# Optimization experiments

Measured on AMD Instinct MI355X. Metric: run time of the kernel, lower is better.

## Reference

```python
import jax, jax.numpy as jnp
import numpy as np

IN_SIZE = 1024
HIDDEN = 1024
BATCH = 4096


def _linear_params(key, out_dim, in_dim):
    # torch nn.Linear init: U(-1/sqrt(in_dim), 1/sqrt(in_dim)) for W and b
    k1, k2 = jax.random.split(key)
    bound = 1.0 / np.sqrt(in_dim)
    W = jax.random.uniform(k1, (out_dim, in_dim), jnp.float32, -bound, bound)
    b = jax.random.uniform(k2, (out_dim,), jnp.float32, -bound, bound)
    return W, b


def setup_inputs() -> dict:
    key = jax.random.key(0)
    keys = jax.random.split(key, 11)
    x = jax.random.normal(keys[0], (BATCH, IN_SIZE), jnp.float32)
    hidden = jax.random.normal(keys[1], (BATCH, HIDDEN), jnp.float32)
    cell = jax.random.normal(keys[2], (BATCH, HIDDEN), jnp.float32)
    names = ['xf', 'xi', 'xo', 'xc', 'hf', 'hi', 'ho', 'hc']
    inp = {'x': x, 'hidden': hidden, 'cell': cell}
    for n, k in zip(names, keys[3:]):
        in_dim = IN_SIZE if n[0] == 'x' else HIDDEN
        W, b = _linear_params(k, HIDDEN, in_dim)
        inp['W_' + n] = W
        inp['b_' + n] = b
    return inp


def reference(x, hidden, cell,
              W_xf, b_xf, W_xi, b_xi, W_xo, b_xo, W_xc, b_xc,
              W_hf, b_hf, W_hi, b_hi, W_ho, b_ho, W_hc, b_hc):
    # gates: sigmoid/tanh over (x-linear + h-linear) pairs
    f = jax.nn.sigmoid(x @ W_xf.T + b_xf + hidden @ W_hf.T + b_hf)
    i = jax.nn.sigmoid(x @ W_xi.T + b_xi + hidden @ W_hi.T + b_hi)
    o = jax.nn.sigmoid(x @ W_xo.T + b_xo + hidden @ W_ho.T + b_ho)
    c = jnp.tanh(x @ W_xc.T + b_xc + hidden @ W_hc.T + b_hc)
    updated_cell = f * cell + i * c
    updated_hidden = o * jnp.tanh(updated_cell)
    return updated_hidden, updated_cell
```

## Files before the change

### kernel.cpp

```cpp
#include <hip/hip_runtime.h>
#include <hip/hip_bf16.h>

#define BATCH 4096
#define NH    1024
#define KCAT  2048
#define NJ    4096
#define NT    (KCAT / 64)

typedef __bf16 bf16x8 __attribute__((ext_vector_type(8)));
typedef float  f32x4  __attribute__((ext_vector_type(4)));
typedef unsigned short u16x8 __attribute__((ext_vector_type(8)));

struct WPtrs { const float* wx[4]; const float* wh[4]; };
struct BPtrs { const float* bx[4]; const float* bh[4]; };

__device__ __forceinline__ unsigned short f2b(float f) {
  union { float f; unsigned u; } v; v.f = f;
  return (unsigned short)((v.u + 0x7fffu + ((v.u >> 16) & 1u)) >> 16);
}

__device__ __forceinline__ void gload_lds16(const void* g, void* l) {
  __builtin_amdgcn_global_load_lds(
      (const __attribute__((address_space(1))) unsigned int*)g,
      (__attribute__((address_space(3))) unsigned int*)l, 16, 0, 0);
}

__device__ __forceinline__ float sigmoid_f(float x) {
  x = fminf(fmaxf(x, -30.f), 30.f);
  return 1.f / (1.f + __expf(-x));
}
__device__ __forceinline__ float tanh_f(float x) {
  x = fminf(fmaxf(x, -15.f), 15.f);
  float e = __expf(2.f * x);
  return (e - 1.f) / (e + 1.f);
}

__global__ __launch_bounds__(256) void pack_all(
    const float* __restrict__ x, const float* __restrict__ h,
    WPtrs W, BPtrs B,
    __hip_bfloat16* __restrict__ Acat, __hip_bfloat16* __restrict__ Bcat,
    float* __restrict__ biasc) {
  int bid = blockIdx.x;
  if (bid < 4096) {
    int t = bid * 256 + threadIdx.x;
    int base = t * 8;
    int row = base >> 11;
    int k   = base & 2047;
    const float* src = (k < 1024) ? (x + (size_t)row * 1024 + k)
                                  : (h + (size_t)row * 1024 + (k - 1024));
    float4 v0 = ((const float4*)src)[0];
    float4 v1 = ((const float4*)src)[1];
    u16x8 o;
    o[0]=f2b(v0.x); o[1]=f2b(v0.y); o[2]=f2b(v0.z); o[3]=f2b(v0.w);
    o[4]=f2b(v1.x); o[5]=f2b(v1.y); o[6]=f2b(v1.z); o[7]=f2b(v1.w);
    *(u16x8*)((unsigned short*)Acat + base) = o;
  } else if (bid < 8192) {
    int t = (bid - 4096) * 256 + threadIdx.x;
    int base = t * 8;
    int j = base >> 11;
    int k = base & 2047;
    int n = ((j >> 6) << 4) + (j & 15);
    int g = (j >> 4) & 3;
    const float* src = (k < 1024) ? (W.wx[g] + (size_t)n * 1024 + k)
                                  : (W.wh[g] + (size_t)n * 1024 + (k - 1024));
    float4 v0 = ((const float4*)src)[0];
    float4 v1 = ((const float4*)src)[1];
    u16x8 o;
    o[0]=f2b(v0.x); o[1]=f2b(v0.y); o[2]=f2b(v0.z); o[3]=f2b(v0.w);
    o[4]=f2b(v1.x); o[5]=f2b(v1.y); o[6]=f2b(v1.z); o[7]=f2b(v1.w);
    *(u16x8*)((unsigned short*)Bcat + base) = o;
  } else {
    int i = (bid - 8192) * 256 + threadIdx.x;
    int g = i >> 10, n = i & 1023;
    biasc[i] = B.bx[g][n] + B.bh[g][n];
  }
}


#define STAGE_A_HALF(T, H)                                                      \
  {                                                                             \
    _Pragma("unroll")                                                           \
    for (int i_ = 0; i_ < 2; ++i_) {                                            \
      gload_lds16(Ag + (size_t)((H)*128 + i_*64 + strow) * KCAT + (T)*64 +      \
                      stchnk * 8,                                               \
                  &smem[((T)&1)*32768 + (H)*8192 + i_*4096 + w*512]);           \
    }                                                                           \
  }
#define STAGE_B_HALF(T, H)                                                      \
  {                                                                             \
    _Pragma("unroll")                                                           \
    for (int i_ = 0; i_ < 2; ++i_) {                                            \
      gload_lds16(Bg + (size_t)((H)*128 + i_*64 + strow) * KCAT + (T)*64 +      \
                      stchnk * 8,                                               \
                  &smem[((T)&1)*32768 + 16384 + (H)*8192 + i_*4096 + w*512]);   \
    }                                                                           \
  }
#define STAGE_A_SLICE(T, S)                                                     \
  {                                                                             \
    gload_lds16(Ag + (size_t)(arbw + (S)*32 + (lane >> 3)) * KCAT + (T)*64 +    \
                    stchnk * 8,                                                 \
                &smem[((T)&1)*32768 + (arbw + (S)*32) * 64]);                   \
  }

__global__ __launch_bounds__(512, 2) void lstm_gemm8(
    const unsigned short* __restrict__ Acat,
    const unsigned short* __restrict__ Bcat,
    const float* __restrict__ biasc,
    const float* __restrict__ cell,
    float* __restrict__ outH, float* __restrict__ outC) {
  __shared__ unsigned short smem[65536];

  const int tid  = threadIdx.x;
  const int w    = tid >> 6;
  const int lane = tid & 63;
  const int wr   = w >> 2;
  const int wc   = w & 3;
  const int lr   = lane & 15;
  const int cb0  = ((lane >> 4) & 3) * 16;
  const int sx   = (lr & 7) << 4;

  const int bid = blockIdx.x;
  const int s   = (bid & 7) * 32 + (bid >> 3);
  const int bx  = s & 15;
  const int by  = s >> 4;

  const unsigned short* Ag = Acat + (size_t)(by * 256) * KCAT;
  const unsigned short* Bg = Bcat + (size_t)(bx * 256) * KCAT;

  const int strow  = w * 8 + (lane >> 3);
  const int stchnk = (lane & 7) ^ ((lane >> 3) & 7);
  const int arbw   = (w >> 2) * 128 + (w & 3) * 8;

  const int arow0 = (wr * 128 + lr) * 128;
  const int brow0 = 32768 + (wc * 64 + lr) * 128;
  const int colb0 = cb0 ^ sx;
  const int colb1 = (64 + cb0) ^ sx;
  const char* smc = (const char*)smem;

  const int n_out = (bx * 4 + wc) * 16 + lr;
  const float bfv = biasc[n_out];
  const float biv = biasc[1024 + n_out];
  const float bov = biasc[2048 + n_out];
  const float bcv = biasc[3072 + n_out];

  f32x4 acc[8][4] = {};

  STAGE_A_HALF(0, 0);
  STAGE_A_HALF(0, 1);
  STAGE_B_HALF(0, 0);
  STAGE_B_HALF(0, 1);
  STAGE_A_SLICE(1, 0);
  STAGE_A_SLICE(1, 1);
  STAGE_A_SLICE(1, 2);
  STAGE_B_HALF(1, 0);
  STAGE_B_HALF(1, 1);
  asm volatile("s_waitcnt vmcnt(7)" ::: "memory");
  __builtin_amdgcn_sched_barrier(0);
  __builtin_amdgcn_s_barrier();

  for (int t = 0; t < NT; ++t) {
    const int cur  = t & 1;
    const int curo = cur * 65536;
    bf16x8 bfr[4][2];
#pragma unroll
    for (int p = 0; p < 4; ++p) {
      bf16x8 af[2][2];
#pragma unroll
      for (int mi = 0; mi < 2; ++mi) {
        af[mi][0] = *(const bf16x8*)(smc + curo + arow0 + (2*p+mi)*2048 + colb0);
        af[mi][1] = *(const bf16x8*)(smc + curo + arow0 + (2*p+mi)*2048 + colb1);
      }
      if (p == 0) {
#pragma unroll
        for (int n = 0; n < 4; ++n) {
          bfr[n][0] = *(const bf16x8*)(smc + curo + brow0 + n*2048 + colb0);
          bfr[n][1] = *(const bf16x8*)(smc + curo + brow0 + n*2048 + colb1);
        }
      }
      if (p == 0 && t + 1 < NT) STAGE_A_SLICE(t + 1, 3);
      if (p == 1 && t + 2 < NT) { STAGE_A_SLICE(t + 2, 0); STAGE_B_HALF(t + 2, 0); }
      if (p == 2 && t + 2 < NT) { STAGE_A_SLICE(t + 2, 1); STAGE_B_HALF(t + 2, 1); }
      if (p == 3 && t + 2 < NT) STAGE_A_SLICE(t + 2, 2);
      if (p == 0) asm volatile("s_waitcnt lgkmcnt(8)" ::: "memory");
      __builtin_amdgcn_sched_barrier(0);
      __builtin_amdgcn_s_barrier();
      asm volatile("s_waitcnt lgkmcnt(0)" ::: "memory");
      __builtin_amdgcn_sched_barrier(0);
      __builtin_amdgcn_s_setprio(1);
#pragma unroll
      for (int mi = 0; mi < 2; ++mi)
#pragma unroll
        for (int n = 0; n < 4; ++n) {
          acc[2*p+mi][n] = __builtin_amdgcn_mfma_f32_16x16x32_bf16(
              af[mi][0], bfr[n][0], acc[2*p+mi][n], 0, 0, 0);
          acc[2*p+mi][n] = __builtin_amdgcn_mfma_f32_16x16x32_bf16(
              af[mi][1], bfr[n][1], acc[2*p+mi][n], 0, 0, 0);
        }
      __builtin_amdgcn_s_setprio(0);
      if (p == 3) {
        if (t < NT - 2) {
          asm volatile("s_waitcnt vmcnt(7)" ::: "memory");
        } else if (t == NT - 2) {
          asm volatile("s_waitcnt vmcnt(0)" ::: "memory");
        }
        __builtin_amdgcn_sched_barrier(0);
      }
      __builtin_amdgcn_s_barrier();
    }
  }

  const int q0 = (lane >> 4) * 4;
#pragma unroll
  for (int m = 0; m < 8; ++m) {
    int row0 = by * 256 + wr * 128 + m * 16 + q0;
#pragma unroll
    for (int q = 0; q < 4; ++q) {
      int row = row0 + q;
      float pf = acc[m][0][q] + bfv;
      float pi = acc[m][1][q] + biv;
      float po = acc[m][2][q] + bov;
      float pc = acc[m][3][q] + bcv;
      float fg = sigmoid_f(pf);
      float ig = sigmoid_f(pi);
      float og = sigmoid_f(po);
      float cg = tanh_f(pc);
      float cold = cell[(size_t)row * NH + n_out];
      float cn = fg * cold + ig * cg;
      float hn = og * tanh_f(cn);
      outH[(size_t)row * NH + n_out] = hn;
      outC[(size_t)row * NH + n_out] = cn;
    }
  }
}

extern "C" void kernel_launch(void* const* d_in, const int* in_sizes, int n_in,
                              void* d_out, int out_size, void* d_ws, size_t ws_size,
                              hipStream_t stream) {
  const float* x    = (const float*)d_in[0];
  const float* h    = (const float*)d_in[1];
  const float* cell = (const float*)d_in[2];
  WPtrs wp; BPtrs bp;
  for (int g = 0; g < 4; ++g) {
    wp.wx[g] = (const float*)d_in[3 + 2 * g];
    bp.bx[g] = (const float*)d_in[4 + 2 * g];
    wp.wh[g] = (const float*)d_in[11 + 2 * g];
    bp.bh[g] = (const float*)d_in[12 + 2 * g];
  }

  char* ws = (char*)d_ws;
  __hip_bfloat16* Acat = (__hip_bfloat16*)ws;
  __hip_bfloat16* Bcat = (__hip_bfloat16*)(ws + (size_t)BATCH * KCAT * 2);
  float* biasc = (float*)(ws + (size_t)BATCH * KCAT * 2 + (size_t)NJ * KCAT * 2);

  float* outH = (float*)d_out;
  float* outC = outH + (size_t)BATCH * NH;

  pack_all<<<8208, 256, 0, stream>>>(x, h, wp, bp, Acat, Bcat, biasc);

  lstm_gemm8<<<256, 512, 0, stream>>>((const unsigned short*)Acat,
                                      (const unsigned short*)Bcat,
                                      biasc, cell, outH, outC);
}
```

Measured before the change: 88.01 us.

## Double-buffer A fragments in registers to overlap LDS reads with MFMA

Adds a two-slot register buffer for A fragments so the next phase's LDS reads are issued before the current phase's MFMAs, including a cross-tile prefetch from the next shared-memory buffer after the barrier. The waitcnt schedule is reworked: the vmcnt wait moves before the last A-slice stage, and lgkmcnt waits now let the prefetch stay in flight. Bias loads move after the main loop to shorten register live ranges. This raises VGPR pressure under 512-thread, 2-block launch bounds, which could cause spills or reduced occupancy.

```diff
diff --git a/kernel.cpp b/kernel.cpp
--- a/kernel.cpp
+++ b/kernel.cpp
@@ -102,6 +102,11 @@
                 &smem[((T)&1)*32768 + (arbw + (S)*32) * 64]);                   \
   }
 
+#define LDA_(BUFO, MP, KH)                                                      \
+  (*(const bf16x8*)(smc + (BUFO) + arow0 + (MP)*2048 + ((KH) ? colb1 : colb0)))
+#define LDB_(BUFO, N, KH)                                                       \
+  (*(const bf16x8*)(smc + (BUFO) + brow0 + (N)*2048 + ((KH) ? colb1 : colb0)))
+
 __global__ __launch_bounds__(512, 2) void lstm_gemm8(
     const unsigned short* __restrict__ Acat,
     const unsigned short* __restrict__ Bcat,
@@ -137,13 +142,9 @@
   const int colb1 = (64 + cb0) ^ sx;
   const char* smc = (const char*)smem;
 
-  const int n_out = (bx * 4 + wc) * 16 + lr;
-  const float bfv = biasc[n_out];
-  const float biv = biasc[1024 + n_out];
-  const float bov = biasc[2048 + n_out];
-  const float bcv = biasc[3072 + n_out];
-
   f32x4 acc[8][4] = {};
+  bf16x8 af[2][2][2];
+  bf16x8 bfr[4][2];
 
   STAGE_A_HALF(0, 0);
   STAGE_A_HALF(0, 1);
@@ -157,34 +158,61 @@
   asm volatile("s_waitcnt vmcnt(7)" ::: "memory");
   __builtin_amdgcn_sched_barrier(0);
   __builtin_amdgcn_s_barrier();
+#pragma unroll
+  for (int mi = 0; mi < 2; ++mi) {
+    af[0][mi][0] = LDA_(0, mi, 0);
+    af[0][mi][1] = LDA_(0, mi, 1);
+  }
 
   for (int t = 0; t < NT; ++t) {
-    const int cur  = t & 1;
-    const int curo = cur * 65536;
-    bf16x8 bfr[4][2];
+    const int curo = (t & 1) * 65536;
+    const int nxto = curo ^ 65536;
 #pragma unroll
     for (int p = 0; p < 4; ++p) {
-      bf16x8 af[2][2];
-#pragma unroll
-      for (int mi = 0; mi < 2; ++mi) {
-        af[mi][0] = *(const bf16x8*)(smc + curo + arow0 + (2*p+mi)*2048 + colb0);
-        af[mi][1] = *(const bf16x8*)(smc + curo + arow0 + (2*p+mi)*2048 + colb1);
-      }
+      const int cs = p & 1;
+      const int ns = cs ^ 1;
       if (p == 0) {
 #pragma unroll
         for (int n = 0; n < 4; ++n) {
-          bfr[n][0] = *(const bf16x8*)(smc + curo + brow0 + n*2048 + colb0);
-          bfr[n][1] = *(const bf16x8*)(smc + curo + brow0 + n*2048 + colb1);
+          bfr[n][0] = LDB_(curo, n, 0);
+          bfr[n][1] = LDB_(curo, n, 1);
+        }
+      }
+      if (p < 3) {
+#pragma unroll
+        for (int mi = 0; mi < 2; ++mi) {
+          af[ns][mi][0] = LDA_(curo, 2*(p+1)+mi, 0);
+          af[ns][mi][1] = LDA_(curo, 2*(p+1)+mi, 1);
         }
       }
       if (p == 0 && t + 1 < NT) STAGE_A_SLICE(t + 1, 3);
       if (p == 1 && t + 2 < NT) { STAGE_A_SLICE(t + 2, 0); STAGE_B_HALF(t + 2, 0); }
       if (p == 2 && t + 2 < NT) { STAGE_A_SLICE(t + 2, 1); STAGE_B_HALF(t + 2, 1); }
-      if (p == 3 && t + 2 < NT) STAGE_A_SLICE(t + 2, 2);
-      if (p == 0) asm volatile("s_waitcnt lgkmcnt(8)" ::: "memory");
+      if (p == 3) {
+        if (t < NT - 2) {
+          asm volatile("s_waitcnt vmcnt(6)" ::: "memory");
+        } else if (t == NT - 2) {
+          asm volatile("s_waitcnt vmcnt(0)" ::: "memory");
+        }
+        __builtin_amdgcn_sched_barrier(0);
+        if (t + 2 < NT) STAGE_A_SLICE(t + 2, 2);
+      }
       __builtin_amdgcn_sched_barrier(0);
       __builtin_amdgcn_s_barrier();
-      asm volatile("s_waitcnt lgkmcnt(0)" ::: "memory");
+      if (p == 3) {
+        if (t + 1 < NT) {
+#pragma unroll
+          for (int mi = 0; mi < 2; ++mi) {
+            af[ns][mi][0] = LDA_(nxto, mi, 0);
+            af[ns][mi][1] = LDA_(nxto, mi, 1);
+          }
+          asm volatile("s_waitcnt lgkmcnt(4)" ::: "memory");
+        } else {
+          asm volatile("s_waitcnt lgkmcnt(0)" ::: "memory");
+        }
+      } else {
+        asm volatile("s_waitcnt lgkmcnt(4)" ::: "memory");
+      }
       __builtin_amdgcn_sched_barrier(0);
       __builtin_amdgcn_s_setprio(1);
 #pragma unroll
@@ -192,24 +220,22 @@
 #pragma unroll
         for (int n = 0; n < 4; ++n) {
           acc[2*p+mi][n] = __builtin_amdgcn_mfma_f32_16x16x32_bf16(
-              af[mi][0], bfr[n][0], acc[2*p+mi][n], 0, 0, 0);
+              af[cs][mi][0], bfr[n][0], acc[2*p+mi][n], 0, 0, 0);
           acc[2*p+mi][n] = __builtin_amdgcn_mfma_f32_16x16x32_bf16(
-              af[mi][1], bfr[n][1], acc[2*p+mi][n], 0, 0, 0);
+              af[cs][mi][1], bfr[n][1], acc[2*p+mi][n], 0, 0, 0);
         }
       __builtin_amdgcn_s_setprio(0);
-      if (p == 3) {
-        if (t < NT - 2) {
-          asm volatile("s_waitcnt vmcnt(7)" ::: "memory");
-        } else if (t == NT - 2) {
-          asm volatile("s_waitcnt vmcnt(0)" ::: "memory");
-        }
-        __builtin_amdgcn_sched_barrier(0);
-      }
       __builtin_amdgcn_s_barrier();
     }
   }
 
+  const int n_out = (bx * 4 + wc) * 16 + lr;
+  const float bfv = biasc[n_out];
+  const float biv = biasc[1024 + n_out];
+  const float bov = biasc[2048 + n_out];
+  const float bcv = biasc[3072 + n_out];
   const int q0 = (lane >> 4) * 4;
+
 #pragma unroll
   for (int m = 0; m < 8; ++m) {
     int row0 = by * 256 + wr * 128 + m * 16 + q0;
```

After: 87.56 us. Within noise of the previous version (-0.5%).

## Software-pipeline LDS fragment loads one phase ahead of MFMAs in GEMM loop

Applied to the files above, without the earlier changes.

Restructures the K-loop so that A fragments for the next quarter are read from LDS while the current quarter's MFMAs run, using a double-buffered af register set and finer lgkmcnt waits. The per-phase barriers and global prefetch issue points are reordered, and the vmcnt threshold moves to match. Bias loads are moved after the main loop to shorten register live ranges. This aims to hide LDS read latency behind matrix math, at the cost of more live VGPRs and a fragile hand-tuned wait schedule.

```diff
diff --git a/kernel.cpp b/kernel.cpp
--- a/kernel.cpp
+++ b/kernel.cpp
@@ -102,6 +102,21 @@
                 &smem[((T)&1)*32768 + (arbw + (S)*32) * 64]);                   \
   }
 
+#define LDA_(BUFO, MP, KH)                                                      \
+  (*(const bf16x8*)(smc + (BUFO) + arow0 + (MP)*2048 + ((KH) ? colb1 : colb0)))
+#define LDB_(BUFO, N, KH)                                                       \
+  (*(const bf16x8*)(smc + (BUFO) + brow0 + (N)*2048 + ((KH) ? colb1 : colb0)))
+
+#define MFMA_HALF(BASE, SET, KH)                                                \
+  {                                                                             \
+    _Pragma("unroll")                                                           \
+    for (int mi_ = 0; mi_ < 2; ++mi_)                                           \
+      _Pragma("unroll")                                                         \
+      for (int n_ = 0; n_ < 4; ++n_)                                            \
+        acc[(BASE)+mi_][n_] = __builtin_amdgcn_mfma_f32_16x16x32_bf16(          \
+            af[SET][mi_][KH], bfr[n_][KH], acc[(BASE)+mi_][n_], 0, 0, 0);       \
+  }
+
 __global__ __launch_bounds__(512, 2) void lstm_gemm8(
     const unsigned short* __restrict__ Acat,
     const unsigned short* __restrict__ Bcat,
@@ -137,13 +152,9 @@
   const int colb1 = (64 + cb0) ^ sx;
   const char* smc = (const char*)smem;
 
-  const int n_out = (bx * 4 + wc) * 16 + lr;
-  const float bfv = biasc[n_out];
-  const float biv = biasc[1024 + n_out];
-  const float bov = biasc[2048 + n_out];
-  const float bcv = biasc[3072 + n_out];
-
   f32x4 acc[8][4] = {};
+  bf16x8 af[2][2][2];
+  bf16x8 bfr[4][2];
 
   STAGE_A_HALF(0, 0);
   STAGE_A_HALF(0, 1);
@@ -159,57 +170,81 @@
   __builtin_amdgcn_s_barrier();
 
   for (int t = 0; t < NT; ++t) {
-    const int cur  = t & 1;
-    const int curo = cur * 65536;
-    bf16x8 bfr[4][2];
-#pragma unroll
-    for (int p = 0; p < 4; ++p) {
-      bf16x8 af[2][2];
-#pragma unroll
-      for (int mi = 0; mi < 2; ++mi) {
-        af[mi][0] = *(const bf16x8*)(smc + curo + arow0 + (2*p+mi)*2048 + colb0);
-        af[mi][1] = *(const bf16x8*)(smc + curo + arow0 + (2*p+mi)*2048 + colb1);
-      }
-      if (p == 0) {
-#pragma unroll
-        for (int n = 0; n < 4; ++n) {
-          bfr[n][0] = *(const bf16x8*)(smc + curo + brow0 + n*2048 + colb0);
-          bfr[n][1] = *(const bf16x8*)(smc + curo + brow0 + n*2048 + colb1);
-        }
-      }
-      if (p == 0 && t + 1 < NT) STAGE_A_SLICE(t + 1, 3);
-      if (p == 1 && t + 2 < NT) { STAGE_A_SLICE(t + 2, 0); STAGE_B_HALF(t + 2, 0); }
-      if (p == 2 && t + 2 < NT) { STAGE_A_SLICE(t + 2, 1); STAGE_B_HALF(t + 2, 1); }
-      if (p == 3 && t + 2 < NT) STAGE_A_SLICE(t + 2, 2);
-      if (p == 0) asm volatile("s_waitcnt lgkmcnt(8)" ::: "memory");
-      __builtin_amdgcn_sched_barrier(0);
-      __builtin_amdgcn_s_barrier();
-      asm volatile("s_waitcnt lgkmcnt(0)" ::: "memory");
-      __builtin_amdgcn_sched_barrier(0);
-      __builtin_amdgcn_s_setprio(1);
-#pragma unroll
-      for (int mi = 0; mi < 2; ++mi)
-#pragma unroll
-        for (int n = 0; n < 4; ++n) {
-          acc[2*p+mi][n] = __builtin_amdgcn_mfma_f32_16x16x32_bf16(
-              af[mi][0], bfr[n][0], acc[2*p+mi][n], 0, 0, 0);
-          acc[2*p+mi][n] = __builtin_amdgcn_mfma_f32_16x16x32_bf16(
-              af[mi][1], bfr[n][1], acc[2*p+mi][n], 0, 0, 0);
-        }
-      __builtin_amdgcn_s_setprio(0);
-      if (p == 3) {
-        if (t < NT - 2) {
-          asm volatile("s_waitcnt vmcnt(7)" ::: "memory");
-        } else if (t == NT - 2) {
-          asm volatile("s_waitcnt vmcnt(0)" ::: "memory");
-        }
-        __builtin_amdgcn_sched_barrier(0);
-      }
-      __builtin_amdgcn_s_barrier();
+    const int curo = (t & 1) * 65536;
+
+    af[0][0][0] = LDA_(curo, 0, 0); af[0][0][1] = LDA_(curo, 0, 1);
+    af[0][1][0] = LDA_(curo, 1, 0); af[0][1][1] = LDA_(curo, 1, 1);
+    __builtin_amdgcn_sched_barrier(0);
+    bfr[0][0] = LDB_(curo, 0, 0); bfr[1][0] = LDB_(curo, 1, 0);
+    bfr[2][0] = LDB_(curo, 2, 0); bfr[3][0] = LDB_(curo, 3, 0);
+    __builtin_amdgcn_sched_barrier(0);
+    bfr[0][1] = LDB_(curo, 0, 1); bfr[1][1] = LDB_(curo, 1, 1);
+    bfr[2][1] = LDB_(curo, 2, 1); bfr[3][1] = LDB_(curo, 3, 1);
+    __builtin_amdgcn_sched_barrier(0);
+    if (t + 1 < NT) STAGE_A_SLICE(t + 1, 3);
+    af[1][0][0] = LDA_(curo, 2, 0); af[1][0][1] = LDA_(curo, 2, 1);
+    af[1][1][0] = LDA_(curo, 3, 0); af[1][1][1] = LDA_(curo, 3, 1);
+    __builtin_amdgcn_sched_barrier(0);
+    __builtin_amdgcn_s_setprio(1);
+    asm volatile("s_waitcnt lgkmcnt(8)" ::: "memory");
+    __builtin_amdgcn_sched_barrier(0);
+    MFMA_HALF(0, 0, 0);
+    asm volatile("s_waitcnt lgkmcnt(4)" ::: "memory");
+    __builtin_amdgcn_sched_barrier(0);
+    MFMA_HALF(0, 0, 1);
+    __builtin_amdgcn_s_setprio(0);
+    __builtin_amdgcn_s_barrier();
+
+    af[0][0][0] = LDA_(curo, 4, 0); af[0][0][1] = LDA_(curo, 4, 1);
+    af[0][1][0] = LDA_(curo, 5, 0); af[0][1][1] = LDA_(curo, 5, 1);
+    __builtin_amdgcn_sched_barrier(0);
+    if (t + 2 < NT) { STAGE_A_SLICE(t + 2, 0); STAGE_B_HALF(t + 2, 0); }
+    __builtin_amdgcn_sched_barrier(0);
+    __builtin_amdgcn_s_setprio(1);
+    asm volatile("s_waitcnt lgkmcnt(4)" ::: "memory");
+    __builtin_amdgcn_sched_barrier(0);
+    MFMA_HALF(2, 1, 0);
+    MFMA_HALF(2, 1, 1);
+    __builtin_amdgcn_s_setprio(0);
+    __builtin_amdgcn_s_barrier();
+
+    af[1][0][0] = LDA_(curo, 6, 0); af[1][0][1] = LDA_(curo, 6, 1);
+    af[1][1][0] = LDA_(curo, 7, 0); af[1][1][1] = LDA_(curo, 7, 1);
+    __builtin_amdgcn_sched_barrier(0);
+    if (t + 2 < NT) { STAGE_A_SLICE(t + 2, 1); STAGE_B_HALF(t + 2, 1); }
+    __builtin_amdgcn_sched_barrier(0);
+    __builtin_amdgcn_s_setprio(1);
+    asm volatile("s_waitcnt lgkmcnt(4)" ::: "memory");
+    __builtin_amdgcn_sched_barrier(0);
+    MFMA_HALF(4, 0, 0);
+    MFMA_HALF(4, 0, 1);
+    __builtin_amdgcn_s_setprio(0);
+    __builtin_amdgcn_s_barrier();
+
+    if (t < NT - 2) {
+      asm volatile("s_waitcnt vmcnt(6)" ::: "memory");
+    } else if (t == NT - 2) {
+      asm volatile("s_waitcnt vmcnt(0)" ::: "memory");
     }
-  }
-
+    __builtin_amdgcn_sched_barrier(0);
+    if (t + 2 < NT) STAGE_A_SLICE(t + 2, 2);
+    __builtin_amdgcn_sched_barrier(0);
+    __builtin_amdgcn_s_setprio(1);
+    asm volatile("s_waitcnt lgkmcnt(0)" ::: "memory");
+    __builtin_amdgcn_sched_barrier(0);
+    MFMA_HALF(6, 1, 0);
+    MFMA_HALF(6, 1, 1);
+    __builtin_amdgcn_s_setprio(0);
+    __builtin_amdgcn_s_barrier();
+  }
+
+  const int n_out = (bx * 4 + wc) * 16 + lr;
+  const float bfv = biasc[n_out];
+  const float biv = biasc[1024 + n_out];
+  const float bov = biasc[2048 + n_out];
+  const float bcv = biasc[3072 + n_out];
   const int q0 = (lane >> 4) * 4;
+
 #pragma unroll
   for (int m = 0; m < 8; ++m) {
     int row0 = by * 256 + wr * 128 + m * 16 + q0;
```

Result: faster. 85.93 us (-2.4%).

## Restructure GEMM main loop into quadrant-based 8-phase ping-pong schedule

Applied to the files above, without the earlier changes.

Replaces the per-k-tile loop of four row-pair phases with a manually unrolled two-tile iteration. Each tile is split into four MFMA quadrants (4 M-fragments by 2 N-fragments), with LDS fragment reads and global-to-LDS staging of A and B halves interleaved between barriers. A is now staged in halves instead of 32-row slices, and the prologue no longer prefetches A for the next tile. The intent is better balance between LDS reads, global loads and MFMA work per barrier phase. In exchange it adds more barriers, a different vmcnt accounting that must be exactly right, and higher register use for the fragment arrays.

```diff
diff --git a/kernel.cpp b/kernel.cpp
--- a/kernel.cpp
+++ b/kernel.cpp
@@ -6,6 +6,7 @@
 #define KCAT  2048
 #define NJ    4096
 #define NT    (KCAT / 64)
+#define NIT   (NT / 2)
 
 typedef __bf16 bf16x8 __attribute__((ext_vector_type(8)));
 typedef float  f32x4  __attribute__((ext_vector_type(4)));
@@ -95,12 +96,47 @@
                   &smem[((T)&1)*32768 + 16384 + (H)*8192 + i_*4096 + w*512]);   \
     }                                                                           \
   }
-#define STAGE_A_SLICE(T, S)                                                     \
-  {                                                                             \
-    gload_lds16(Ag + (size_t)(arbw + (S)*32 + (lane >> 3)) * KCAT + (T)*64 +    \
-                    stchnk * 8,                                                 \
-                &smem[((T)&1)*32768 + (arbw + (S)*32) * 64]);                   \
-  }
+
+#define READ_A(BUFO, MQ)                                                        \
+  {                                                                             \
+    _Pragma("unroll")                                                           \
+    for (int mf_ = 0; mf_ < 4; ++mf_) {                                         \
+      af[mf_][0] = *(const bf16x8*)(smc + (BUFO) + arow0 +                      \
+                                    ((MQ)*4 + mf_)*2048 + colb0);               \
+      af[mf_][1] = *(const bf16x8*)(smc + (BUFO) + arow0 +                      \
+                                    ((MQ)*4 + mf_)*2048 + colb1);               \
+    }                                                                           \
+  }
+#define READ_B(BUFO, NQ)                                                        \
+  {                                                                             \
+    _Pragma("unroll")                                                           \
+    for (int nf_ = 0; nf_ < 2; ++nf_) {                                         \
+      bfr[NQ][nf_][0] = *(const bf16x8*)(smc + (BUFO) + brow0 +                 \
+                                         ((NQ)*2 + nf_)*2048 + colb0);          \
+      bfr[NQ][nf_][1] = *(const bf16x8*)(smc + (BUFO) + brow0 +                 \
+                                         ((NQ)*2 + nf_)*2048 + colb1);          \
+    }                                                                           \
+  }
+#define MFMA_Q(MQ, NQ)                                                          \
+  {                                                                             \
+    _Pragma("unroll")                                                           \
+    for (int ks_ = 0; ks_ < 2; ++ks_)                                           \
+      _Pragma("unroll")                                                         \
+      for (int mf_ = 0; mf_ < 4; ++mf_)                                         \
+        _Pragma("unroll")                                                       \
+        for (int nf_ = 0; nf_ < 2; ++nf_)                                       \
+          acc[(MQ)*4 + mf_][(NQ)*2 + nf_] =                                     \
+              __builtin_amdgcn_mfma_f32_16x16x32_bf16(                          \
+                  af[mf_][ks_], bfr[NQ][nf_][ks_],                              \
+                  acc[(MQ)*4 + mf_][(NQ)*2 + nf_], 0, 0, 0);                    \
+  }
+
+#define BAR    __builtin_amdgcn_s_barrier()
+#define LGKM0  { asm volatile("s_waitcnt lgkmcnt(0)" ::: "memory");             \
+                 __builtin_amdgcn_sched_barrier(0); }
+#define LGKM8  asm volatile("s_waitcnt lgkmcnt(8)" ::: "memory")
+#define PRIO1  __builtin_amdgcn_s_setprio(1)
+#define PRIO0  __builtin_amdgcn_s_setprio(0)
 
 __global__ __launch_bounds__(512, 2) void lstm_gemm8(
     const unsigned short* __restrict__ Acat,
@@ -129,7 +165,6 @@
 
   const int strow  = w * 8 + (lane >> 3);
   const int stchnk = (lane & 7) ^ ((lane >> 3) & 7);
-  const int arbw   = (w >> 2) * 128 + (w & 3) * 8;
 
   const int arow0 = (wr * 128 + lr) * 128;
   const int brow0 = 32768 + (wc * 64 + lr) * 128;
@@ -137,79 +172,86 @@
   const int colb1 = (64 + cb0) ^ sx;
   const char* smc = (const char*)smem;
 
+  f32x4 acc[8][4] = {};
+  bf16x8 af[4][2];
+  bf16x8 bfr[2][2][2];
+
+  STAGE_A_HALF(0, 0);
+  STAGE_A_HALF(0, 1);
+  STAGE_B_HALF(0, 0);
+  STAGE_B_HALF(0, 1);
+  STAGE_B_HALF(1, 0);
+  STAGE_B_HALF(1, 1);
+  asm volatile("s_waitcnt vmcnt(4)" ::: "memory");
+  __builtin_amdgcn_sched_barrier(0);
+  BAR;
+
+  for (int it = 0; it < NIT; ++it) {
+    const int t0 = 2 * it;
+    const bool full = (t0 + 2 < NT);
+
+    READ_A(0, 0);
+    READ_B(0, 0);
+    STAGE_A_HALF(t0 + 1, 0);
+    LGKM8;
+    BAR; LGKM0;
+    PRIO1; MFMA_Q(0, 0); PRIO0;
+    BAR;
+    READ_B(0, 1);
+    STAGE_A_HALF(t0 + 1, 1);
+    BAR; LGKM0;
+    PRIO1; MFMA_Q(0, 1); PRIO0;
+    BAR;
+    READ_A(0, 1);
+    if (full) STAGE_B_HALF(t0 + 2, 0);
+    BAR; LGKM0;
+    PRIO1; MFMA_Q(1, 0); PRIO0;
+    BAR;
+    if (full) {
+      STAGE_B_HALF(t0 + 2, 1);
+      asm volatile("s_waitcnt vmcnt(4)" ::: "memory");
+    } else {
+      asm volatile("s_waitcnt vmcnt(0)" ::: "memory");
+    }
+    __builtin_amdgcn_sched_barrier(0);
+    BAR; LGKM0;
+    PRIO1; MFMA_Q(1, 1); PRIO0;
+    BAR;
+
+    READ_A(65536, 0);
+    READ_B(65536, 0);
+    if (full) STAGE_A_HALF(t0 + 2, 0);
+    LGKM8;
+    BAR; LGKM0;
+    PRIO1; MFMA_Q(0, 0); PRIO0;
+    BAR;
+    READ_B(65536, 1);
+    if (full) STAGE_A_HALF(t0 + 2, 1);
+    BAR; LGKM0;
+    PRIO1; MFMA_Q(0, 1); PRIO0;
+    BAR;
+    READ_A(65536, 1);
+    if (full) STAGE_B_HALF(t0 + 3, 0);
+    BAR; LGKM0;
+    PRIO1; MFMA_Q(1, 0); PRIO0;
+    BAR;
+    if (full) {
+      STAGE_B_HALF(t0 + 3, 1);
+      asm volatile("s_waitcnt vmcnt(4)" ::: "memory");
+      __builtin_amdgcn_sched_barrier(0);
+    }
+    BAR; LGKM0;
+    PRIO1; MFMA_Q(1, 1); PRIO0;
+    BAR;
+  }
+
   const int n_out = (bx * 4 + wc) * 16 + lr;
   const float bfv = biasc[n_out];
   const float biv = biasc[1024 + n_out];
   const float bov = biasc[2048 + n_out];
   const float bcv = biasc[3072 + n_out];
-
-  f32x4 acc[8][4] = {};
-
-  STAGE_A_HALF(0, 0);
-  STAGE_A_HALF(0, 1);
-  STAGE_B_HALF(0, 0);
-  STAGE_B_HALF(0, 1);
-  STAGE_A_SLICE(1, 0);
-  STAGE_A_SLICE(1, 1);
-  STAGE_A_SLICE(1, 2);
-  STAGE_B_HALF(1, 0);
-  STAGE_B_HALF(1, 1);
-  asm volatile("s_waitcnt vmcnt(7)" ::: "memory");
-  __builtin_amdgcn_sched_barrier(0);
-  __builtin_amdgcn_s_barrier();
-
-  for (int t = 0; t < NT; ++t) {
-    const int cur  = t & 1;
-    const int curo = cur * 65536;
-    bf16x8 bfr[4][2];
-#pragma unroll
-    for (int p = 0; p < 4; ++p) {
-      bf16x8 af[2][2];
-#pragma unroll
-      for (int mi = 0; mi < 2; ++mi) {
-        af[mi][0] = *(const bf16x8*)(smc + curo + arow0 + (2*p+mi)*2048 + colb0);
-        af[mi][1] = *(const bf16x8*)(smc + curo + arow0 + (2*p+mi)*2048 + colb1);
-      }
-      if (p == 0) {
-#pragma unroll
-        for (int n = 0; n < 4; ++n) {
-          bfr[n][0] = *(const bf16x8*)(smc + curo + brow0 + n*2048 + colb0);
-          bfr[n][1] = *(const bf16x8*)(smc + curo + brow0 + n*2048 + colb1);
-        }
-      }
-      if (p == 0 && t + 1 < NT) STAGE_A_SLICE(t + 1, 3);
-      if (p == 1 && t + 2 < NT) { STAGE_A_SLICE(t + 2, 0); STAGE_B_HALF(t + 2, 0); }
-      if (p == 2 && t + 2 < NT) { STAGE_A_SLICE(t + 2, 1); STAGE_B_HALF(t + 2, 1); }
-      if (p == 3 && t + 2 < NT) STAGE_A_SLICE(t + 2, 2);
-      if (p == 0) asm volatile("s_waitcnt lgkmcnt(8)" ::: "memory");
-      __builtin_amdgcn_sched_barrier(0);
-      __builtin_amdgcn_s_barrier();
-      asm volatile("s_waitcnt lgkmcnt(0)" ::: "memory");
-      __builtin_amdgcn_sched_barrier(0);
-      __builtin_amdgcn_s_setprio(1);
-#pragma unroll
-      for (int mi = 0; mi < 2; ++mi)
-#pragma unroll
-        for (int n = 0; n < 4; ++n) {
-          acc[2*p+mi][n] = __builtin_amdgcn_mfma_f32_16x16x32_bf16(
-              af[mi][0], bfr[n][0], acc[2*p+mi][n], 0, 0, 0);
-          acc[2*p+mi][n] = __builtin_amdgcn_mfma_f32_16x16x32_bf16(
-              af[mi][1], bfr[n][1], acc[2*p+mi][n], 0, 0, 0);
-        }
-      __builtin_amdgcn_s_setprio(0);
-      if (p == 3) {
-        if (t < NT - 2) {
-          asm volatile("s_waitcnt vmcnt(7)" ::: "memory");
-        } else if (t == NT - 2) {
-          asm volatile("s_waitcnt vmcnt(0)" ::: "memory");
-        }
-        __builtin_amdgcn_sched_barrier(0);
-      }
-      __builtin_amdgcn_s_barrier();
-    }
-  }
-
   const int q0 = (lane >> 4) * 4;
+
 #pragma unroll
   for (int m = 0; m < 8; ++m) {
     int row0 = by * 256 + wr * 128 + m * 16 + q0;
```

Result: faster. 85.69 us (-2.6%).
